# Kernel optimization log

Measured on AMD Instinct MI355X. Metric: run time of the kernel, lower is better.

Reference implementation:

```python
import jax, jax.numpy as jnp
import numpy as np

ALPHA = 1.0
GAMMA = 2.0            # initial_focal_gamma (epoch 0)
DIST_THRESHOLD = 0.1
WEIGHT_FACTOR = 2.0
DISTANCE_WEIGHT = 1.0


def setup_inputs() -> dict:
    key = jax.random.key(0)
    k1, k2, k3, k4 = jax.random.split(key, 4)
    B, N, C, M = 64, 16384, 6, 128
    inputs = jax.random.normal(k1, (B, N), dtype=jnp.float32)
    targets = (jax.random.uniform(k2, (B, N)) < 0.05).astype(jnp.float32)
    point_coords = jax.random.uniform(k3, (B, N, C), dtype=jnp.float32)
    corner_coords = jax.random.uniform(k4, (B, M, 3), dtype=jnp.float32)
    # mark last 32 corners per sample invalid (sentinel -1), exercising the mask
    invalid = jnp.arange(M) >= (M - 32)
    corner_coords = jnp.where(invalid[None, :, None], -1.0, corner_coords)
    return {"inputs": inputs, "targets": targets,
            "point_coords": point_coords, "corner_coords": corner_coords}


def _bce_with_logits(logits, targets):
    # stable: max(x,0) - x*t + log(1+exp(-|x|))
    return jnp.maximum(logits, 0.0) - logits * targets + jnp.log1p(jnp.exp(-jnp.abs(logits)))


def _focal_elementwise(inputs, targets):
    ce = _bce_with_logits(inputs, targets)
    probs = jax.nn.sigmoid(inputs)
    p_t = probs * targets + (1.0 - probs) * (1.0 - targets)
    return ALPHA * (1.0 - p_t) ** GAMMA * ce  # [B, N]


def reference(inputs, targets, point_coords, corner_coords):
    # focal loss (mean reduction)
    focal_elem = _focal_elementwise(inputs, targets)
    focal_loss = focal_elem.mean()

    # distance-weighted loss: 1-NN distance from each point to valid corners
    pts = point_coords[..., :3]                          # [B, N, 3]
    valid = corner_coords[..., 0] > -1.0                 # [B, M]
    pts_sq = jnp.sum(pts * pts, axis=-1)                 # [B, N]
    cor_sq = jnp.sum(corner_coords * corner_coords, axis=-1)  # [B, M]
    cross = jnp.einsum('bnc,bmc->bnm', pts, corner_coords)    # [B, N, M]
    d2 = pts_sq[:, :, None] + cor_sq[:, None, :] - 2.0 * cross
    d2 = jnp.maximum(d2, 1e-12)
    d2 = jnp.where(valid[:, None, :], d2, jnp.inf)       # mask invalid corners
    min_d = jnp.sqrt(jnp.min(d2, axis=-1))               # [B, N]; inf if no valid corners
    dist_w = jnp.exp(-min_d / DIST_THRESHOLD)            # 0 when min_d = inf
    weights = 1.0 + WEIGHT_FACTOR * dist_w
    distance_loss = (focal_elem * weights).mean()

    total_loss = focal_loss + DISTANCE_WEIGHT * distance_loss
    return total_loss, focal_loss, distance_loss
```

## Files before the change

kernel.cpp:

```cpp
#include <hip/hip_runtime.h>
#include <math.h>

typedef float f32x2 __attribute__((ext_vector_type(2)));

#define BLOCK 256
#define PPT 8
#define MCOR 128
constexpr int Bb = 64;
constexpr int Nn = 16384;
constexpr int GRIDX = Nn / (BLOCK * PPT);
constexpr int NPART = GRIDX * Bb;

static __device__ __forceinline__ f32x2 splat2(float s) { return f32x2{s, s}; }

__global__ __launch_bounds__(BLOCK) void acl_main(
    const float* __restrict__ inputs,
    const float* __restrict__ targets,
    const float* __restrict__ pts,
    const float* __restrict__ corners,
    float2* __restrict__ partials)
{
    __shared__ float4 cs[MCOR];
    __shared__ float2 wsum[BLOCK / 64];

    const int b   = blockIdx.y;
    const int tid = threadIdx.x;

    if (tid < MCOR) {
        const float* c = corners + ((size_t)b * MCOR + tid) * 3;
        float cx = c[0], cy = c[1], cz = c[2];
        float csq = (cx > -1.0f) ? (cx*cx + cy*cy + cz*cz) : __builtin_inff();
        cs[tid] = make_float4(-2.0f*cx, -2.0f*cy, -2.0f*cz, csq);
    }
    __syncthreads();

    const int n0 = blockIdx.x * (BLOCK * PPT) + tid * PPT;
    const size_t base = (size_t)b * Nn + n0;

    const float4* xv = (const float4*)(inputs  + base);
    const float4* tv = (const float4*)(targets + base);
    const float4* pv = (const float4*)(pts + base * 6);
    const float4 x0 = xv[0], x1 = xv[1];
    const float4 t0v = tv[0], t1v = tv[1];
    float4 v[12];
    #pragma unroll
    for (int k = 0; k < 12; ++k) v[k] = pv[k];

    const float pxs[PPT] = {v[0].x, v[1].z, v[3].x, v[4].z, v[6].x, v[7].z, v[9].x, v[10].z};
    const float pys[PPT] = {v[0].y, v[1].w, v[3].y, v[4].w, v[6].y, v[7].w, v[9].y, v[10].w};
    const float pzs[PPT] = {v[0].z, v[2].x, v[3].z, v[5].x, v[6].z, v[8].x, v[9].z, v[11].x};

    f32x2 PX[4], PY[4], PZ[4], dmin[4];
    #pragma unroll
    for (int q = 0; q < 4; ++q) {
        PX[q] = f32x2{pxs[2*q], pxs[2*q+1]};
        PY[q] = f32x2{pys[2*q], pys[2*q+1]};
        PZ[q] = f32x2{pzs[2*q], pzs[2*q+1]};
        dmin[q] = splat2(__builtin_inff());
    }

    #pragma unroll 4
    for (int m = 0; m < MCOR; m += 2) {
        const float4 c0 = cs[m];
        const float4 c1 = cs[m + 1];
        #pragma unroll
        for (int q = 0; q < 4; ++q) {
            f32x2 u0 = __builtin_elementwise_fma(splat2(c0.x), PX[q],
                       __builtin_elementwise_fma(splat2(c0.y), PY[q],
                       __builtin_elementwise_fma(splat2(c0.z), PZ[q], splat2(c0.w))));
            f32x2 u1 = __builtin_elementwise_fma(splat2(c1.x), PX[q],
                       __builtin_elementwise_fma(splat2(c1.y), PY[q],
                       __builtin_elementwise_fma(splat2(c1.z), PZ[q], splat2(c1.w))));
            dmin[q] = __builtin_elementwise_min(dmin[q],
                      __builtin_elementwise_min(u0, u1));
        }
    }

    const float dm[PPT] = {dmin[0].x, dmin[0].y, dmin[1].x, dmin[1].y,
                           dmin[2].x, dmin[2].y, dmin[3].x, dmin[3].y};
    const float xs[PPT] = {x0.x, x0.y, x0.z, x0.w, x1.x, x1.y, x1.z, x1.w};
    const float ts[PPT] = {t0v.x, t0v.y, t0v.z, t0v.w, t1v.x, t1v.y, t1v.z, t1v.w};

    float fs = 0.0f, ds = 0.0f;
    #pragma unroll
    for (int j = 0; j < PPT; ++j) {
        float psq = fmaf(pxs[j], pxs[j], fmaf(pys[j], pys[j], pzs[j]*pzs[j]));
        float d2  = fmaxf(psq + dm[j], 1e-12f);
        float md  = sqrtf(d2);
        float w   = fmaf(2.0f, __expf(-10.0f * md), 1.0f);

        float x = xs[j], t = ts[j];
        float ax = fabsf(x);
        float ce = fmaxf(x, 0.0f) - x*t + __logf(1.0f + __expf(-ax));
        float p  = 1.0f / (1.0f + __expf(-x));
        float pt = p*t + (1.0f - p)*(1.0f - t);
        float om = 1.0f - pt;
        float fe = om * om * ce;

        fs += fe;
        ds = fmaf(fe, w, ds);
    }

    #pragma unroll
    for (int off = 32; off > 0; off >>= 1) {
        fs += __shfl_down(fs, off, 64);
        ds += __shfl_down(ds, off, 64);
    }
    const int wave = tid >> 6, lane = tid & 63;
    if (lane == 0) wsum[wave] = make_float2(fs, ds);
    __syncthreads();
    if (tid == 0) {
        float F = 0.0f, D = 0.0f;
        #pragma unroll
        for (int w = 0; w < BLOCK / 64; ++w) { F += wsum[w].x; D += wsum[w].y; }
        partials[(size_t)blockIdx.y * gridDim.x + blockIdx.x] = make_float2(F, D);
    }
}

__global__ __launch_bounds__(256) void acl_final(
    const float2* __restrict__ partials, float* __restrict__ out)
{
    double f = 0.0, d = 0.0;
    for (int i = threadIdx.x; i < NPART; i += 256) {
        float2 p = partials[i];
        f += (double)p.x;
        d += (double)p.y;
    }
    #pragma unroll
    for (int off = 32; off > 0; off >>= 1) {
        f += __shfl_down(f, off, 64);
        d += __shfl_down(d, off, 64);
    }
    __shared__ double sf[4], sd[4];
    const int wave = threadIdx.x >> 6, lane = threadIdx.x & 63;
    if (lane == 0) { sf[wave] = f; sd[wave] = d; }
    __syncthreads();
    if (threadIdx.x == 0) {
        double F = sf[0] + sf[1] + sf[2] + sf[3];
        double D = sd[0] + sd[1] + sd[2] + sd[3];
        double inv = 1.0 / ((double)Bb * (double)Nn);
        float focal = (float)(F * inv);
        float dist  = (float)(D * inv);
        out[0] = focal + dist;
        out[1] = focal;
        out[2] = dist;
    }
}

extern "C" void kernel_launch(void* const* d_in, const int* in_sizes, int n_in,
                              void* d_out, int out_size, void* d_ws, size_t ws_size,
                              hipStream_t stream) {
    const float* inputs  = (const float*)d_in[0];
    const float* targets = (const float*)d_in[1];
    const float* pts     = (const float*)d_in[2];
    const float* corners = (const float*)d_in[3];
    float* out = (float*)d_out;
    float2* partials = (float2*)d_ws;

    dim3 grid(GRIDX, Bb);
    acl_main<<<grid, BLOCK, 0, stream>>>(inputs, targets, pts, corners, partials);
    acl_final<<<1, 256, 0, stream>>>(partials, out);
}
```

Baseline: 21.60 us.

## Fuse main and final reduction kernels via cooperative launch with grid sync

Merges the per-block partial computation and the final reduction into one cooperative kernel that uses a grid-wide barrier, with block 0 doing the final sum. The aim is to remove the second kernel launch and its launch gap. The grid is flattened to 1D (512 blocks) and launch_bounds requests two blocks per SM so all blocks can be co-resident. If the cooperative launch fails, it falls back to the original two-kernel path. A grid barrier has its own cost, and cooperative launch can add overhead.

```diff
diff --git a/kernel.cpp b/kernel.cpp
--- a/kernel.cpp
+++ b/kernel.cpp
@@ -1,5 +1,8 @@
 #include <hip/hip_runtime.h>
+#include <hip/hip_cooperative_groups.h>
 #include <math.h>
+
+namespace cg = cooperative_groups;
 
 typedef float f32x2 __attribute__((ext_vector_type(2)));
 
@@ -9,22 +12,23 @@
 constexpr int Bb = 64;
 constexpr int Nn = 16384;
 constexpr int GRIDX = Nn / (BLOCK * PPT);
-constexpr int NPART = GRIDX * Bb;
+constexpr int NBLK  = GRIDX * Bb;
 
 static __device__ __forceinline__ f32x2 splat2(float s) { return f32x2{s, s}; }
 
-__global__ __launch_bounds__(BLOCK) void acl_main(
+static __device__ __forceinline__ void compute_partial(
     const float* __restrict__ inputs,
     const float* __restrict__ targets,
     const float* __restrict__ pts,
     const float* __restrict__ corners,
-    float2* __restrict__ partials)
+    float2* __restrict__ partials,
+    int bid, int tid)
 {
     __shared__ float4 cs[MCOR];
     __shared__ float2 wsum[BLOCK / 64];
 
-    const int b   = blockIdx.y;
-    const int tid = threadIdx.x;
+    const int b  = bid / GRIDX;
+    const int gx = bid % GRIDX;
 
     if (tid < MCOR) {
         const float* c = corners + ((size_t)b * MCOR + tid) * 3;
@@ -34,7 +38,7 @@
     }
     __syncthreads();
 
-    const int n0 = blockIdx.x * (BLOCK * PPT) + tid * PPT;
+    const int n0 = gx * (BLOCK * PPT) + tid * PPT;
     const size_t base = (size_t)b * Nn + n0;
 
     const float4* xv = (const float4*)(inputs  + base);
@@ -113,16 +117,17 @@
         float F = 0.0f, D = 0.0f;
         #pragma unroll
         for (int w = 0; w < BLOCK / 64; ++w) { F += wsum[w].x; D += wsum[w].y; }
-        partials[(size_t)blockIdx.y * gridDim.x + blockIdx.x] = make_float2(F, D);
-    }
-}
-
-__global__ __launch_bounds__(256) void acl_final(
-    const float2* __restrict__ partials, float* __restrict__ out)
+        partials[bid] = make_float2(F, D);
+    }
+}
+
+static __device__ __forceinline__ void finalize(
+    const float2* __restrict__ partials, float* __restrict__ out, int tid)
 {
     double f = 0.0, d = 0.0;
-    for (int i = threadIdx.x; i < NPART; i += 256) {
-        float2 p = partials[i];
+    #pragma unroll
+    for (int k = 0; k < NBLK / BLOCK; ++k) {
+        float2 p = partials[tid + k * BLOCK];
         f += (double)p.x;
         d += (double)p.y;
     }
@@ -131,20 +136,50 @@
         f += __shfl_down(f, off, 64);
         d += __shfl_down(d, off, 64);
     }
-    __shared__ double sf[4], sd[4];
-    const int wave = threadIdx.x >> 6, lane = threadIdx.x & 63;
+    __shared__ double sf[BLOCK / 64], sd[BLOCK / 64];
+    const int wave = tid >> 6, lane = tid & 63;
     if (lane == 0) { sf[wave] = f; sd[wave] = d; }
     __syncthreads();
-    if (threadIdx.x == 0) {
-        double F = sf[0] + sf[1] + sf[2] + sf[3];
-        double D = sd[0] + sd[1] + sd[2] + sd[3];
-        double inv = 1.0 / ((double)Bb * (double)Nn);
+    if (tid == 0) {
+        double F = 0.0, D = 0.0;
+        #pragma unroll
+        for (int w = 0; w < BLOCK / 64; ++w) { F += sf[w]; D += sd[w]; }
+        const double inv = 1.0 / ((double)Bb * (double)Nn);
         float focal = (float)(F * inv);
         float dist  = (float)(D * inv);
         out[0] = focal + dist;
         out[1] = focal;
         out[2] = dist;
     }
+}
+
+__global__ __launch_bounds__(BLOCK, 2) void acl_coop(
+    const float* __restrict__ inputs,
+    const float* __restrict__ targets,
+    const float* __restrict__ pts,
+    const float* __restrict__ corners,
+    float2* __restrict__ partials,
+    float* __restrict__ out)
+{
+    compute_partial(inputs, targets, pts, corners, partials, blockIdx.x, threadIdx.x);
+    cg::this_grid().sync();
+    if (blockIdx.x == 0) finalize(partials, out, threadIdx.x);
+}
+
+__global__ __launch_bounds__(BLOCK) void acl_main(
+    const float* __restrict__ inputs,
+    const float* __restrict__ targets,
+    const float* __restrict__ pts,
+    const float* __restrict__ corners,
+    float2* __restrict__ partials)
+{
+    compute_partial(inputs, targets, pts, corners, partials, blockIdx.x, threadIdx.x);
+}
+
+__global__ __launch_bounds__(BLOCK) void acl_final(
+    const float2* __restrict__ partials, float* __restrict__ out)
+{
+    finalize(partials, out, threadIdx.x);
 }
 
 extern "C" void kernel_launch(void* const* d_in, const int* in_sizes, int n_in,
@@ -157,7 +192,15 @@
     float* out = (float*)d_out;
     float2* partials = (float2*)d_ws;
 
-    dim3 grid(GRIDX, Bb);
-    acl_main<<<grid, BLOCK, 0, stream>>>(inputs, targets, pts, corners, partials);
-    acl_final<<<1, 256, 0, stream>>>(partials, out);
-}
+    void* args[] = { (void*)&inputs, (void*)&targets, (void*)&pts, (void*)&corners,
+                     (void*)&partials, (void*)&out };
+    hipError_t err = hipLaunchCooperativeKernel((void*)acl_coop,
+                                                dim3(NBLK), dim3(BLOCK),
+                                                args, 0, stream);
+    if (err != hipSuccess) {
+        (void)hipGetLastError();
+        acl_main<<<dim3(NBLK), dim3(BLOCK), 0, stream>>>(inputs, targets, pts,
+                                                         corners, partials);
+        acl_final<<<1, dim3(BLOCK), 0, stream>>>(partials, out);
+    }
+}
```

New measurement: 56.36 us. +160.9%, slower.
